# Kernel tuning notes

Hardware: AMD Instinct MI355X
Metric: run time of the kernel (lower is better)

Reference implementation:

```python
import jax, jax.numpy as jnp
import numpy as np

N_NODES = 100000
N_EDGES = 1250000
D_IN = 64
D_H = 64
D_OUT = 32


def setup_inputs() -> dict:
    key = jax.random.key(0)
    ks = jax.random.split(key, 8)
    x = jax.random.normal(ks[0], (N_NODES, D_IN), dtype=jnp.float32)
    edge_index = jax.random.randint(ks[1], (2, N_EDGES), 0, N_NODES, dtype=jnp.int64)
    s = 0.1
    W1_l = jax.random.normal(ks[2], (D_H, D_IN), dtype=jnp.float32) * s
    W1_r = jax.random.normal(ks[3], (D_H, D_IN), dtype=jnp.float32) * s
    b1 = jnp.zeros((D_H,), dtype=jnp.float32)
    W2_l = jax.random.normal(ks[4], (D_OUT, D_H), dtype=jnp.float32) * s
    W2_r = jax.random.normal(ks[5], (D_OUT, D_H), dtype=jnp.float32) * s
    b2 = jnp.zeros((D_OUT,), dtype=jnp.float32)
    return {"x": x, "edge_index": edge_index, "W1_l": W1_l, "W1_r": W1_r,
            "b1": b1, "W2_l": W2_l, "W2_r": W2_r, "b2": b2}


def _sage_conv(x, src, dst, W_l, W_r, b):
    # PyG SAGEConv (aggr='mean', root_weight=True):
    #   out = lin_l(mean_{j in N(i)} x_j) + lin_r(x_i)
    n = x.shape[0]
    msg = x[src]                                            # [E, d] gather
    ssum = jax.ops.segment_sum(msg, dst, num_segments=n)    # [N, d]
    deg = jax.ops.segment_sum(jnp.ones((src.shape[0], 1), x.dtype), dst,
                              num_segments=n)               # [N, 1]
    mean = ssum / jnp.maximum(deg, 1.0)
    return mean @ W_l.T + b + x @ W_r.T


def reference(x, edge_index, W1_l, W1_r, b1, W2_l, W2_r, b2):
    src = edge_index[0]
    dst = edge_index[1]
    h = jax.nn.relu(_sage_conv(x, src, dst, W1_l, W1_r, b1))
    out = _sage_conv(h, src, dst, W2_l, W2_r, b2)
    return out
```

## Files before the change

kernel.cpp:

```cpp
#include <hip/hip_runtime.h>

#define N_NODES 100000
#define N_EDGES 1250000
#define D_IN 64
#define D_H 64
#define D_OUT 32

#define BUCKETS 196
#define GRP 512
#define PREP_NB 512
#define PREP_CH 2442
#define SCAP 48
#define BSTRIDE (PREP_NB*SCAP)
#define CSRCAP 8192

#define XS 6.0f
#define HS 5.0f

typedef __attribute__((ext_vector_type(8))) short bf16x8;
typedef __attribute__((ext_vector_type(4))) float f32x4;

__device__ __forceinline__ unsigned short f2bf(float f) {
    unsigned u = __float_as_uint(f);
    u = (u + 0x7fffu + ((u >> 16) & 1u)) >> 16;
    return (unsigned short)u;
}
__device__ __forceinline__ float bfhi(unsigned v) { return __uint_as_float(v & 0xffff0000u); }
__device__ __forceinline__ float bflo(unsigned v) { return __uint_as_float(v << 16); }


__global__ __launch_bounds__(256) void k_prep(const float* __restrict__ x,
                                              unsigned* __restrict__ xq,
                                              const int* __restrict__ src,
                                              const int* __restrict__ dst,
                                              int* __restrict__ ebuf,
                                              int* __restrict__ pcnt) {
    __shared__ int ofs[BUCKETS];
    int t = threadIdx.x, b = blockIdx.x;
    for (int i = t; i < BUCKETS; i += 256) ofs[i] = 0;
    __syncthreads();

    const float QS = 127.0f / XS;
    const int TOT = N_NODES * 64 / 4;
    for (int i = b * 256 + t; i < TOT; i += PREP_NB * 256) {
        float4 v = *(const float4*)(x + (size_t)i * 4);
        float c0 = fminf(fmaxf(v.x, -XS), XS);
        float c1 = fminf(fmaxf(v.y, -XS), XS);
        float c2 = fminf(fmaxf(v.z, -XS), XS);
        float c3 = fminf(fmaxf(v.w, -XS), XS);
        unsigned q0 = (unsigned)((int)rintf(c0 * QS) + 128);
        unsigned q1 = (unsigned)((int)rintf(c1 * QS) + 128);
        unsigned q2 = (unsigned)((int)rintf(c2 * QS) + 128);
        unsigned q3 = (unsigned)((int)rintf(c3 * QS) + 128);
        xq[i] = q0 | (q1 << 8) | (q2 << 16) | (q3 << 24);
    }

    int e0 = b * PREP_CH;
    int e1 = e0 + PREP_CH; if (e1 > N_EDGES) e1 = N_EDGES;
    for (int e = e0 + t; e < e1; e += 256) {
        int s = src[e], d = dst[e];
        if ((unsigned)d >= N_NODES) continue;
        int sv = ((unsigned)s < N_NODES) ? s : 0;
        int bk = d >> 9;
        int r = atomicAdd(&ofs[bk], 1);
        if (r < SCAP) ebuf[bk * BSTRIDE + b * SCAP + r] = ((d & 511) << 17) | sv;
    }
    __syncthreads();
    for (int i = t; i < BUCKETS; i += 256) {
        int v = ofs[i]; if (v > SCAP) v = SCAP;
        pcnt[i * PREP_NB + b] = v;
    }
}

__global__ __launch_bounds__(512) void k_phb(const int* __restrict__ ebuf,
                                             const int* __restrict__ pcnt,
                                             int2* __restrict__ rd,
                                             int* __restrict__ csr_src) {
    __shared__ int sedge[CSRCAP];
    __shared__ int cnt[GRP];
    __shared__ int wsum[8];
    int b = blockIdx.x, t = threadIdx.x;
    int lane = t & 63, w = t >> 6;

    cnt[t] = 0;
    int c = pcnt[b * PREP_NB + t];

    int run = c;
    #pragma unroll
    for (int off = 1; off < 64; off <<= 1) {
        int u = __shfl_up(run, off, 64);
        if (lane >= off) run += u;
    }
    if (lane == 63) wsum[w] = run;
    __syncthreads();
    int wbase = 0, tot = 0;
    #pragma unroll
    for (int i = 0; i < 8; ++i) { int v = wsum[i]; tot += v; if (i < w) wbase += v; }
    int base = wbase + run - c;
    int n = tot; if (n > CSRCAP) n = CSRCAP;

    {
        const int4* sp4 = (const int4*)(ebuf + (size_t)b * BSTRIDE + (size_t)t * SCAP);
        for (int j = 0; j < c; j += 4) {
            int4 v = sp4[j >> 2];
            int p = base + j;
            if (p + 0 < CSRCAP)              sedge[p + 0] = v.x;
            if (j + 1 < c && p + 1 < CSRCAP) sedge[p + 1] = v.y;
            if (j + 2 < c && p + 2 < CSRCAP) sedge[p + 2] = v.z;
            if (j + 3 < c && p + 3 < CSRCAP) sedge[p + 3] = v.w;
        }
    }
    __syncthreads();
    for (int i = t; i < n; i += 512) atomicAdd(&cnt[sedge[i] >> 17], 1);
    __syncthreads();

    int d = cnt[t];
    int rund = d;
    #pragma unroll
    for (int off = 1; off < 64; off <<= 1) {
        int u = __shfl_up(rund, off, 64);
        if (lane >= off) rund += u;
    }
    if (lane == 63) wsum[w] = rund;
    __syncthreads();
    int wb2 = 0;
    #pragma unroll
    for (int i = 0; i < 8; ++i) { if (i < w) wb2 += wsum[i]; }
    int gabs = b * CSRCAP + wb2 + rund - d;
    int node = b * GRP + t;
    if (node < N_NODES) rd[node] = make_int2(gabs, d);
    cnt[t] = gabs;
    __syncthreads();
    for (int i = t; i < n; i += 512) {
        int v = sedge[i];
        int pos = atomicAdd(&cnt[v >> 17], 1);
        csr_src[pos] = v & 0x1FFFF;
    }
}

__global__ __launch_bounds__(256) void k_gather1(
    const unsigned* __restrict__ xq,
    const int2* __restrict__ rd, const int* __restrict__ csr_src,
    uint4* __restrict__ meanh)
{
    int lane = threadIdx.x & 63;
    int wv = threadIdx.x >> 6;
    int c = lane & 7;
    int gb = lane & 56;
    const uint2* xp = (const uint2*)xq;

    int node0 = blockIdx.x * 32 + wv * 8 + (gb >> 3);
    for (int row = node0; row < N_NODES; row += gridDim.x * 32) {
        int2 rdv = rd[row];
        int start = rdv.x, dg = rdv.y;
        int end = start + dg;
        unsigned aL0=0, aH0=0, aL1=0, aH1=0;
        unsigned bL0=0, bH0=0, bL1=0, bH1=0;
        unsigned cL0=0, cH0=0, cL1=0, cH1=0;
        unsigned dL0=0, dH0=0, dL1=0, dH1=0;
        for (int eb = start; eb < end; eb += 8) {
            int nv = end - eb; if (nv > 8) nv = 8;
            int sid = (c < nv) ? csr_src[eb + c] : 0;
            int j = 0;
            for (; j + 4 <= nv; j += 4) {
                int s0 = __shfl(sid, gb + j + 0, 64);
                int s1 = __shfl(sid, gb + j + 1, 64);
                int s2 = __shfl(sid, gb + j + 2, 64);
                int s3 = __shfl(sid, gb + j + 3, 64);
                uint2 v0 = xp[(size_t)s0 * 8 + c];
                uint2 v1 = xp[(size_t)s1 * 8 + c];
                uint2 v2 = xp[(size_t)s2 * 8 + c];
                uint2 v3 = xp[(size_t)s3 * 8 + c];
                aL0 += v0.x & 0x00FF00FFu; aH0 += (v0.x >> 8) & 0x00FF00FFu;
                aL1 += v0.y & 0x00FF00FFu; aH1 += (v0.y >> 8) & 0x00FF00FFu;
                bL0 += v1.x & 0x00FF00FFu; bH0 += (v1.x >> 8) & 0x00FF00FFu;
                bL1 += v1.y & 0x00FF00FFu; bH1 += (v1.y >> 8) & 0x00FF00FFu;
                cL0 += v2.x & 0x00FF00FFu; cH0 += (v2.x >> 8) & 0x00FF00FFu;
                cL1 += v2.y & 0x00FF00FFu; cH1 += (v2.y >> 8) & 0x00FF00FFu;
                dL0 += v3.x & 0x00FF00FFu; dH0 += (v3.x >> 8) & 0x00FF00FFu;
                dL1 += v3.y & 0x00FF00FFu; dH1 += (v3.y >> 8) & 0x00FF00FFu;
            }
            for (; j < nv; ++j) {
                int s0 = __shfl(sid, gb + j, 64);
                uint2 v0 = xp[(size_t)s0 * 8 + c];
                aL0 += v0.x & 0x00FF00FFu; aH0 += (v0.x >> 8) & 0x00FF00FFu;
                aL1 += v0.y & 0x00FF00FFu; aH1 += (v0.y >> 8) & 0x00FF00FFu;
            }
        }
        unsigned L0 = (aL0 + bL0) + (cL0 + dL0);
        unsigned H0 = (aH0 + bH0) + (cH0 + dH0);
        unsigned L1 = (aL1 + bL1) + (cL1 + dL1);
        unsigned H1 = (aH1 + bH1) + (cH1 + dH1);
        float fd = (float)dg;
        float rdeg = 1.0f / fmaxf(fd, 1.0f);
        const float SC = XS / 127.0f;
        float base = -128.0f * fd;
        float m0 = ((float)(L0 & 0xFFFFu) + base) * SC * rdeg;
        float m1 = ((float)(H0 & 0xFFFFu) + base) * SC * rdeg;
        float m2 = ((float)(L0 >> 16)    + base) * SC * rdeg;
        float m3 = ((float)(H0 >> 16)    + base) * SC * rdeg;
        float m4 = ((float)(L1 & 0xFFFFu) + base) * SC * rdeg;
        float m5 = ((float)(H1 & 0xFFFFu) + base) * SC * rdeg;
        float m6 = ((float)(L1 >> 16)    + base) * SC * rdeg;
        float m7 = ((float)(H1 >> 16)    + base) * SC * rdeg;
        uint4 o;
        o.x = (unsigned)f2bf(m0) | ((unsigned)f2bf(m1) << 16);
        o.y = (unsigned)f2bf(m2) | ((unsigned)f2bf(m3) << 16);
        o.z = (unsigned)f2bf(m4) | ((unsigned)f2bf(m5) << 16);
        o.w = (unsigned)f2bf(m6) | ((unsigned)f2bf(m7) << 16);
        meanh[(size_t)row * 8 + c] = o;
    }
}

__global__ __launch_bounds__(256) void k_gemm1(
    const float* __restrict__ x, const unsigned short* __restrict__ meanh,
    const float* __restrict__ W1l, const float* __restrict__ W1r,
    const float* __restrict__ b1,
    const float* __restrict__ W2l, const float* __restrict__ W2r,
    unsigned char* __restrict__ hq, unsigned short* __restrict__ hrh)
{
    __shared__ short sWB1[4 * 4 * 64 * 8];
    __shared__ short sWB2[2 * 4 * 64 * 8];
    __shared__ short htile[4][16 * 72];

    int tid = threadIdx.x;
    for (int e = tid; e < 1024; e += 256) {
        int kc = e >> 8, nt = (e >> 6) & 3, ln = e & 63;
        int cc = ln & 15, qd = ln >> 4;
        int n = nt * 16 + cc, k0 = kc * 32 + qd * 8;
        const float* sp = (k0 < 64) ? (W1l + n * 64 + k0) : (W1r + n * 64 + (k0 - 64));
        short* dp = sWB1 + e * 8;
        #pragma unroll
        for (int j = 0; j < 8; ++j) dp[j] = (short)f2bf(sp[j]);
    }
    for (int e = tid; e < 512; e += 256) {
        int kc = e >> 8, nt = (e >> 6) & 3, ln = e & 63;
        int cc = ln & 15, qd = ln >> 4;
        int n = nt * 16 + cc, k0 = kc * 32 + qd * 8;
        const float* sp = (n < 32) ? (W2l + n * 64 + k0) : (W2r + (n - 32) * 64 + k0);
        short* dp = sWB2 + e * 8;
        #pragma unroll
        for (int j = 0; j < 8; ++j) dp[j] = (short)f2bf(sp[j]);
    }
    __syncthreads();

    int lane = tid & 63, w = tid >> 6;
    int c = lane & 15, quad = lane >> 4;
    float bias[4];
    #pragma unroll
    for (int nt = 0; nt < 4; ++nt) bias[nt] = b1[nt * 16 + c];

    const bf16x8* B1 = (const bf16x8*)sWB1;
    const bf16x8* B2 = (const bf16x8*)sWB2;
    short* ht = htile[w];
    const float HQS = 127.0f / HS;

    for (int r0 = blockIdx.x * 64 + w * 16; r0 < N_NODES; r0 += gridDim.x * 64) {
        int ra = r0 + c; if (ra > N_NODES - 1) ra = N_NODES - 1;
        const bf16x8* mrow = (const bf16x8*)(meanh + (size_t)ra * 64);
        const float4* xr = (const float4*)(x + (size_t)ra * 64);
        bf16x8 a0 = mrow[quad];
        bf16x8 a1 = mrow[4 + quad];
        float4 f0 = xr[quad * 2 + 0];
        float4 f1 = xr[quad * 2 + 1];
        float4 f2 = xr[8 + quad * 2 + 0];
        float4 f3 = xr[8 + quad * 2 + 1];
        bf16x8 a2, a3;
        a2[0] = (short)f2bf(f0.x); a2[1] = (short)f2bf(f0.y);
        a2[2] = (short)f2bf(f0.z); a2[3] = (short)f2bf(f0.w);
        a2[4] = (short)f2bf(f1.x); a2[5] = (short)f2bf(f1.y);
        a2[6] = (short)f2bf(f1.z); a2[7] = (short)f2bf(f1.w);
        a3[0] = (short)f2bf(f2.x); a3[1] = (short)f2bf(f2.y);
        a3[2] = (short)f2bf(f2.z); a3[3] = (short)f2bf(f2.w);
        a3[4] = (short)f2bf(f3.x); a3[5] = (short)f2bf(f3.y);
        a3[6] = (short)f2bf(f3.z); a3[7] = (short)f2bf(f3.w);

        f32x4 acc[4];
        #pragma unroll
        for (int nt = 0; nt < 4; ++nt) acc[nt] = (f32x4){0.f, 0.f, 0.f, 0.f};
        #pragma unroll
        for (int nt = 0; nt < 4; ++nt)
            acc[nt] = __builtin_amdgcn_mfma_f32_16x16x32_bf16(a0, B1[(0 * 4 + nt) * 64 + lane], acc[nt], 0, 0, 0);
        #pragma unroll
        for (int nt = 0; nt < 4; ++nt)
            acc[nt] = __builtin_amdgcn_mfma_f32_16x16x32_bf16(a1, B1[(1 * 4 + nt) * 64 + lane], acc[nt], 0, 0, 0);
        #pragma unroll
        for (int nt = 0; nt < 4; ++nt)
            acc[nt] = __builtin_amdgcn_mfma_f32_16x16x32_bf16(a2, B1[(2 * 4 + nt) * 64 + lane], acc[nt], 0, 0, 0);
        #pragma unroll
        for (int nt = 0; nt < 4; ++nt)
            acc[nt] = __builtin_amdgcn_mfma_f32_16x16x32_bf16(a3, B1[(3 * 4 + nt) * 64 + lane], acc[nt], 0, 0, 0);

        #pragma unroll
        for (int nt = 0; nt < 4; ++nt) {
            #pragma unroll
            for (int reg = 0; reg < 4; ++reg) {
                float hv = fmaxf(acc[nt][reg] + bias[nt], 0.0f);
                ht[(quad * 4 + reg) * 72 + nt * 16 + c] = (short)f2bf(hv);
            }
        }
        bf16x8 h0 = *(const bf16x8*)(ht + c * 72 + 0  + quad * 8);
        bf16x8 h1 = *(const bf16x8*)(ht + c * 72 + 32 + quad * 8);

        f32x4 acc2[4];
        #pragma unroll
        for (int nt = 0; nt < 4; ++nt) acc2[nt] = (f32x4){0.f, 0.f, 0.f, 0.f};
        #pragma unroll
        for (int nt = 0; nt < 4; ++nt)
            acc2[nt] = __builtin_amdgcn_mfma_f32_16x16x32_bf16(h0, B2[(0 * 4 + nt) * 64 + lane], acc2[nt], 0, 0, 0);
        #pragma unroll
        for (int nt = 0; nt < 4; ++nt)
            acc2[nt] = __builtin_amdgcn_mfma_f32_16x16x32_bf16(h1, B2[(1 * 4 + nt) * 64 + lane], acc2[nt], 0, 0, 0);

        #pragma unroll
        for (int reg = 0; reg < 4; ++reg) {
            int row = r0 + quad * 4 + reg;
            if (row < N_NODES) {
                float c0v = fminf(fmaxf(acc2[0][reg], -HS), HS);
                float c1v = fminf(fmaxf(acc2[1][reg], -HS), HS);
                unsigned q0 = (unsigned)((int)rintf(c0v * HQS) + 128);
                unsigned q1 = (unsigned)((int)rintf(c1v * HQS) + 128);
                hq[(size_t)row * 32 + c]      = (unsigned char)q0;
                hq[(size_t)row * 32 + 16 + c] = (unsigned char)q1;
                hrh[(size_t)row * 32 + c]      = f2bf(acc2[2][reg]);
                hrh[(size_t)row * 32 + 16 + c] = f2bf(acc2[3][reg]);
            }
        }
    }
}

__global__ __launch_bounds__(256) void k_l2(
    const unsigned char* __restrict__ hq,
    const unsigned short* __restrict__ hrh,
    const int2* __restrict__ rd, const int* __restrict__ csr_src,
    const float* __restrict__ b2, float* __restrict__ out)
{
    int lane = threadIdx.x & 63;
    int wv = threadIdx.x >> 6;
    int cc = lane & 3;
    int gb = lane & 60;
    const uint2* hp = (const uint2*)hq;
    const uint4* hrp = (const uint4*)hrh;
    float4 b2v0 = ((const float4*)b2)[cc * 2 + 0];
    float4 b2v1 = ((const float4*)b2)[cc * 2 + 1];

    int node0 = blockIdx.x * 64 + wv * 16 + (gb >> 2);
    for (int row = node0; row < N_NODES; row += gridDim.x * 64) {
        int2 rdv = rd[row];
        int start = rdv.x, dg = rdv.y;
        int end = start + dg;
        unsigned aL0=0, aH0=0, aL1=0, aH1=0;
        unsigned bL0=0, bH0=0, bL1=0, bH1=0;
        unsigned cL0=0, cH0=0, cL1=0, cH1=0;
        unsigned dL0=0, dH0=0, dL1=0, dH1=0;
        for (int eb = start; eb < end; eb += 4) {
            int nv = end - eb; if (nv > 4) nv = 4;
            int sid = (cc < nv) ? csr_src[eb + cc] : 0;
            if (nv == 4) {
                int s0 = __shfl(sid, gb + 0, 64);
                int s1 = __shfl(sid, gb + 1, 64);
                int s2 = __shfl(sid, gb + 2, 64);
                int s3 = __shfl(sid, gb + 3, 64);
                uint2 v0 = hp[(size_t)s0 * 4 + cc];
                uint2 v1 = hp[(size_t)s1 * 4 + cc];
                uint2 v2 = hp[(size_t)s2 * 4 + cc];
                uint2 v3 = hp[(size_t)s3 * 4 + cc];
                aL0 += v0.x & 0x00FF00FFu; aH0 += (v0.x >> 8) & 0x00FF00FFu;
                aL1 += v0.y & 0x00FF00FFu; aH1 += (v0.y >> 8) & 0x00FF00FFu;
                bL0 += v1.x & 0x00FF00FFu; bH0 += (v1.x >> 8) & 0x00FF00FFu;
                bL1 += v1.y & 0x00FF00FFu; bH1 += (v1.y >> 8) & 0x00FF00FFu;
                cL0 += v2.x & 0x00FF00FFu; cH0 += (v2.x >> 8) & 0x00FF00FFu;
                cL1 += v2.y & 0x00FF00FFu; cH1 += (v2.y >> 8) & 0x00FF00FFu;
                dL0 += v3.x & 0x00FF00FFu; dH0 += (v3.x >> 8) & 0x00FF00FFu;
                dL1 += v3.y & 0x00FF00FFu; dH1 += (v3.y >> 8) & 0x00FF00FFu;
            } else {
                for (int j = 0; j < nv; ++j) {
                    int s0 = __shfl(sid, gb + j, 64);
                    uint2 v0 = hp[(size_t)s0 * 4 + cc];
                    aL0 += v0.x & 0x00FF00FFu; aH0 += (v0.x >> 8) & 0x00FF00FFu;
                    aL1 += v0.y & 0x00FF00FFu; aH1 += (v0.y >> 8) & 0x00FF00FFu;
                }
            }
        }
        unsigned L0 = (aL0 + bL0) + (cL0 + dL0);
        unsigned H0 = (aH0 + bH0) + (cH0 + dH0);
        unsigned L1 = (aL1 + bL1) + (cL1 + dL1);
        unsigned H1 = (aH1 + bH1) + (cH1 + dH1);
        float fd = (float)dg;
        float rdeg = 1.0f / fmaxf(fd, 1.0f);
        const float SC = HS / 127.0f;
        float base = -128.0f * fd;
        uint4 hru = hrp[(size_t)row * 4 + cc];
        float4 o0, o1;
        o0.x = ((float)(L0 & 0xFFFFu) + base) * SC * rdeg + (bflo(hru.x) + b2v0.x);
        o0.y = ((float)(H0 & 0xFFFFu) + base) * SC * rdeg + (bfhi(hru.x) + b2v0.y);
        o0.z = ((float)(L0 >> 16)     + base) * SC * rdeg + (bflo(hru.y) + b2v0.z);
        o0.w = ((float)(H0 >> 16)     + base) * SC * rdeg + (bfhi(hru.y) + b2v0.w);
        o1.x = ((float)(L1 & 0xFFFFu) + base) * SC * rdeg + (bflo(hru.z) + b2v1.x);
        o1.y = ((float)(H1 & 0xFFFFu) + base) * SC * rdeg + (bfhi(hru.z) + b2v1.y);
        o1.z = ((float)(L1 >> 16)     + base) * SC * rdeg + (bflo(hru.w) + b2v1.z);
        o1.w = ((float)(H1 >> 16)     + base) * SC * rdeg + (bfhi(hru.w) + b2v1.w);
        ((float4*)out)[(size_t)row * 8 + cc * 2 + 0] = o0;
        ((float4*)out)[(size_t)row * 8 + cc * 2 + 1] = o1;
    }
}

extern "C" void kernel_launch(void* const* d_in, const int* in_sizes, int n_in,
                              void* d_out, int out_size, void* d_ws, size_t ws_size,
                              hipStream_t stream) {
    const float* x   = (const float*)d_in[0];
    const int*   ei  = (const int*)d_in[1];
    const float* W1l = (const float*)d_in[2];
    const float* W1r = (const float*)d_in[3];
    const float* b1  = (const float*)d_in[4];
    const float* W2l = (const float*)d_in[5];
    const float* W2r = (const float*)d_in[6];
    const float* b2  = (const float*)d_in[7];
    float* out = (float*)d_out;

    const int* src = ei;
    const int* dst = ei + N_EDGES;

    char* w = (char*)d_ws;
    int2* rd     = (int2*)w;  w += sizeof(int2) * (N_NODES + 4);
    int* pcnt    = (int*)w;   w += sizeof(int) * (PREP_NB * BUCKETS);
    int* csr_src = (int*)w;   w += sizeof(int) * (BUCKETS * CSRCAP);
    int* ebuf    = (int*)w;   w += sizeof(int) * ((size_t)BUCKETS * BSTRIDE);
    unsigned*       xq   = (unsigned*)w;       w += sizeof(int)   * (size_t)N_NODES * 16;
    unsigned*       meanh  = (unsigned*)w;     w += sizeof(int)   * (size_t)N_NODES * 32;
    unsigned char*  hq   = (unsigned char*)w;  w += (size_t)N_NODES * 32;
    unsigned short* hrh  = (unsigned short*)w;

    k_prep<<<PREP_NB, 256, 0, stream>>>(x, xq, src, dst, ebuf, pcnt);
    k_phb<<<BUCKETS, 512, 0, stream>>>(ebuf, pcnt, rd, csr_src);
    k_gather1<<<3125, 256, 0, stream>>>(xq, rd, csr_src, (uint4*)meanh);
    k_gemm1<<<1024, 256, 0, stream>>>(
        x, (const unsigned short*)meanh, W1l, W1r, b1, W2l, W2r, hq, hrh);
    k_l2<<<1563, 256, 0, stream>>>(hq, hrh, rd, csr_src, b2, out);
}
```

Before: 173.2 us.

## Fuse layer-1 neighbor gather into the layer-1 GEMM kernel via LDS tile

Merges the separate gather kernel into the GEMM kernel. Each wave now gathers the int8 neighbor features for its 16 rows, 4 lanes per row with 16-byte loads, and writes the bf16 mean into its LDS tile, where the MFMA A operands are read. This drops the global round trip for the mean buffer and one kernel launch. In exchange, gather parallelism falls from 3125 blocks to 1024 persistent blocks with fewer loads in flight per row, so latency hiding for the irregular gather may suffer.

```diff
diff --git a/kernel.cpp b/kernel.cpp
--- a/kernel.cpp
+++ b/kernel.cpp
@@ -138,82 +138,9 @@
     }
 }
 
-__global__ __launch_bounds__(256) void k_gather1(
-    const unsigned* __restrict__ xq,
+__global__ __launch_bounds__(256) void k_gg(
+    const float* __restrict__ x, const unsigned* __restrict__ xq,
     const int2* __restrict__ rd, const int* __restrict__ csr_src,
-    uint4* __restrict__ meanh)
-{
-    int lane = threadIdx.x & 63;
-    int wv = threadIdx.x >> 6;
-    int c = lane & 7;
-    int gb = lane & 56;
-    const uint2* xp = (const uint2*)xq;
-
-    int node0 = blockIdx.x * 32 + wv * 8 + (gb >> 3);
-    for (int row = node0; row < N_NODES; row += gridDim.x * 32) {
-        int2 rdv = rd[row];
-        int start = rdv.x, dg = rdv.y;
-        int end = start + dg;
-        unsigned aL0=0, aH0=0, aL1=0, aH1=0;
-        unsigned bL0=0, bH0=0, bL1=0, bH1=0;
-        unsigned cL0=0, cH0=0, cL1=0, cH1=0;
-        unsigned dL0=0, dH0=0, dL1=0, dH1=0;
-        for (int eb = start; eb < end; eb += 8) {
-            int nv = end - eb; if (nv > 8) nv = 8;
-            int sid = (c < nv) ? csr_src[eb + c] : 0;
-            int j = 0;
-            for (; j + 4 <= nv; j += 4) {
-                int s0 = __shfl(sid, gb + j + 0, 64);
-                int s1 = __shfl(sid, gb + j + 1, 64);
-                int s2 = __shfl(sid, gb + j + 2, 64);
-                int s3 = __shfl(sid, gb + j + 3, 64);
-                uint2 v0 = xp[(size_t)s0 * 8 + c];
-                uint2 v1 = xp[(size_t)s1 * 8 + c];
-                uint2 v2 = xp[(size_t)s2 * 8 + c];
-                uint2 v3 = xp[(size_t)s3 * 8 + c];
-                aL0 += v0.x & 0x00FF00FFu; aH0 += (v0.x >> 8) & 0x00FF00FFu;
-                aL1 += v0.y & 0x00FF00FFu; aH1 += (v0.y >> 8) & 0x00FF00FFu;
-                bL0 += v1.x & 0x00FF00FFu; bH0 += (v1.x >> 8) & 0x00FF00FFu;
-                bL1 += v1.y & 0x00FF00FFu; bH1 += (v1.y >> 8) & 0x00FF00FFu;
-                cL0 += v2.x & 0x00FF00FFu; cH0 += (v2.x >> 8) & 0x00FF00FFu;
-                cL1 += v2.y & 0x00FF00FFu; cH1 += (v2.y >> 8) & 0x00FF00FFu;
-                dL0 += v3.x & 0x00FF00FFu; dH0 += (v3.x >> 8) & 0x00FF00FFu;
-                dL1 += v3.y & 0x00FF00FFu; dH1 += (v3.y >> 8) & 0x00FF00FFu;
-            }
-            for (; j < nv; ++j) {
-                int s0 = __shfl(sid, gb + j, 64);
-                uint2 v0 = xp[(size_t)s0 * 8 + c];
-                aL0 += v0.x & 0x00FF00FFu; aH0 += (v0.x >> 8) & 0x00FF00FFu;
-                aL1 += v0.y & 0x00FF00FFu; aH1 += (v0.y >> 8) & 0x00FF00FFu;
-            }
-        }
-        unsigned L0 = (aL0 + bL0) + (cL0 + dL0);
-        unsigned H0 = (aH0 + bH0) + (cH0 + dH0);
-        unsigned L1 = (aL1 + bL1) + (cL1 + dL1);
-        unsigned H1 = (aH1 + bH1) + (cH1 + dH1);
-        float fd = (float)dg;
-        float rdeg = 1.0f / fmaxf(fd, 1.0f);
-        const float SC = XS / 127.0f;
-        float base = -128.0f * fd;
-        float m0 = ((float)(L0 & 0xFFFFu) + base) * SC * rdeg;
-        float m1 = ((float)(H0 & 0xFFFFu) + base) * SC * rdeg;
-        float m2 = ((float)(L0 >> 16)    + base) * SC * rdeg;
-        float m3 = ((float)(H0 >> 16)    + base) * SC * rdeg;
-        float m4 = ((float)(L1 & 0xFFFFu) + base) * SC * rdeg;
-        float m5 = ((float)(H1 & 0xFFFFu) + base) * SC * rdeg;
-        float m6 = ((float)(L1 >> 16)    + base) * SC * rdeg;
-        float m7 = ((float)(H1 >> 16)    + base) * SC * rdeg;
-        uint4 o;
-        o.x = (unsigned)f2bf(m0) | ((unsigned)f2bf(m1) << 16);
-        o.y = (unsigned)f2bf(m2) | ((unsigned)f2bf(m3) << 16);
-        o.z = (unsigned)f2bf(m4) | ((unsigned)f2bf(m5) << 16);
-        o.w = (unsigned)f2bf(m6) | ((unsigned)f2bf(m7) << 16);
-        meanh[(size_t)row * 8 + c] = o;
-    }
-}
-
-__global__ __launch_bounds__(256) void k_gemm1(
-    const float* __restrict__ x, const unsigned short* __restrict__ meanh,
     const float* __restrict__ W1l, const float* __restrict__ W1r,
     const float* __restrict__ b1,
     const float* __restrict__ W2l, const float* __restrict__ W2r,
@@ -246,21 +173,102 @@
 
     int lane = tid & 63, w = tid >> 6;
     int c = lane & 15, quad = lane >> 4;
+    int gl = lane & 3, gb = lane & 60, gr = lane >> 2;
     float bias[4];
     #pragma unroll
     for (int nt = 0; nt < 4; ++nt) bias[nt] = b1[nt * 16 + c];
 
     const bf16x8* B1 = (const bf16x8*)sWB1;
     const bf16x8* B2 = (const bf16x8*)sWB2;
+    const uint4* xp4 = (const uint4*)xq;
     short* ht = htile[w];
     const float HQS = 127.0f / HS;
+    const float SC = XS / 127.0f;
 
     for (int r0 = blockIdx.x * 64 + w * 16; r0 < N_NODES; r0 += gridDim.x * 64) {
+        {
+            int grow = r0 + gr;
+            int2 rdv = rd[(grow < N_NODES) ? grow : (N_NODES - 1)];
+            int start = rdv.x;
+            int dg = (grow < N_NODES) ? rdv.y : 0;
+            int end = start + dg;
+            unsigned L0=0,H0=0,L1=0,H1=0,L2=0,H2=0,L3=0,H3=0;
+            for (int eb = start; eb < end; eb += 4) {
+                int nv = end - eb; if (nv > 4) nv = 4;
+                int sid = (gl < nv) ? csr_src[eb + gl] : 0;
+                if (nv == 4) {
+                    int s0 = __shfl(sid, gb + 0, 64);
+                    int s1 = __shfl(sid, gb + 1, 64);
+                    int s2 = __shfl(sid, gb + 2, 64);
+                    int s3 = __shfl(sid, gb + 3, 64);
+                    uint4 v0 = xp4[(size_t)s0 * 4 + gl];
+                    uint4 v1 = xp4[(size_t)s1 * 4 + gl];
+                    uint4 v2 = xp4[(size_t)s2 * 4 + gl];
+                    uint4 v3 = xp4[(size_t)s3 * 4 + gl];
+                    L0 += v0.x & 0x00FF00FFu; H0 += (v0.x >> 8) & 0x00FF00FFu;
+                    L1 += v0.y & 0x00FF00FFu; H1 += (v0.y >> 8) & 0x00FF00FFu;
+                    L2 += v0.z & 0x00FF00FFu; H2 += (v0.z >> 8) & 0x00FF00FFu;
+                    L3 += v0.w & 0x00FF00FFu; H3 += (v0.w >> 8) & 0x00FF00FFu;
+                    L0 += v1.x & 0x00FF00FFu; H0 += (v1.x >> 8) & 0x00FF00FFu;
+                    L1 += v1.y & 0x00FF00FFu; H1 += (v1.y >> 8) & 0x00FF00FFu;
+                    L2 += v1.z & 0x00FF00FFu; H2 += (v1.z >> 8) & 0x00FF00FFu;
+                    L3 += v1.w & 0x00FF00FFu; H3 += (v1.w >> 8) & 0x00FF00FFu;
+                    L0 += v2.x & 0x00FF00FFu; H0 += (v2.x >> 8) & 0x00FF00FFu;
+                    L1 += v2.y & 0x00FF00FFu; H1 += (v2.y >> 8) & 0x00FF00FFu;
+                    L2 += v2.z & 0x00FF00FFu; H2 += (v2.z >> 8) & 0x00FF00FFu;
+                    L3 += v2.w & 0x00FF00FFu; H3 += (v2.w >> 8) & 0x00FF00FFu;
+                    L0 += v3.x & 0x00FF00FFu; H0 += (v3.x >> 8) & 0x00FF00FFu;
+                    L1 += v3.y & 0x00FF00FFu; H1 += (v3.y >> 8) & 0x00FF00FFu;
+                    L2 += v3.z & 0x00FF00FFu; H2 += (v3.z >> 8) & 0x00FF00FFu;
+                    L3 += v3.w & 0x00FF00FFu; H3 += (v3.w >> 8) & 0x00FF00FFu;
+                } else {
+                    for (int j = 0; j < nv; ++j) {
+                        int s0 = __shfl(sid, gb + j, 64);
+                        uint4 v0 = xp4[(size_t)s0 * 4 + gl];
+                        L0 += v0.x & 0x00FF00FFu; H0 += (v0.x >> 8) & 0x00FF00FFu;
+                        L1 += v0.y & 0x00FF00FFu; H1 += (v0.y >> 8) & 0x00FF00FFu;
+                        L2 += v0.z & 0x00FF00FFu; H2 += (v0.z >> 8) & 0x00FF00FFu;
+                        L3 += v0.w & 0x00FF00FFu; H3 += (v0.w >> 8) & 0x00FF00FFu;
+                    }
+                }
+            }
+            float fd = (float)dg;
+            float rdeg = 1.0f / fmaxf(fd, 1.0f);
+            float base = -128.0f * fd;
+            float m0  = ((float)(L0 & 0xFFFFu) + base) * SC * rdeg;
+            float m1  = ((float)(H0 & 0xFFFFu) + base) * SC * rdeg;
+            float m2  = ((float)(L0 >> 16)     + base) * SC * rdeg;
+            float m3  = ((float)(H0 >> 16)     + base) * SC * rdeg;
+            float m4  = ((float)(L1 & 0xFFFFu) + base) * SC * rdeg;
+            float m5  = ((float)(H1 & 0xFFFFu) + base) * SC * rdeg;
+            float m6  = ((float)(L1 >> 16)     + base) * SC * rdeg;
+            float m7  = ((float)(H1 >> 16)     + base) * SC * rdeg;
+            float m8  = ((float)(L2 & 0xFFFFu) + base) * SC * rdeg;
+            float m9  = ((float)(H2 & 0xFFFFu) + base) * SC * rdeg;
+            float m10 = ((float)(L2 >> 16)     + base) * SC * rdeg;
+            float m11 = ((float)(H2 >> 16)     + base) * SC * rdeg;
+            float m12 = ((float)(L3 & 0xFFFFu) + base) * SC * rdeg;
+            float m13 = ((float)(H3 & 0xFFFFu) + base) * SC * rdeg;
+            float m14 = ((float)(L3 >> 16)     + base) * SC * rdeg;
+            float m15 = ((float)(H3 >> 16)     + base) * SC * rdeg;
+            uint4 o0, o1;
+            o0.x = (unsigned)f2bf(m0)  | ((unsigned)f2bf(m1)  << 16);
+            o0.y = (unsigned)f2bf(m2)  | ((unsigned)f2bf(m3)  << 16);
+            o0.z = (unsigned)f2bf(m4)  | ((unsigned)f2bf(m5)  << 16);
+            o0.w = (unsigned)f2bf(m6)  | ((unsigned)f2bf(m7)  << 16);
+            o1.x = (unsigned)f2bf(m8)  | ((unsigned)f2bf(m9)  << 16);
+            o1.y = (unsigned)f2bf(m10) | ((unsigned)f2bf(m11) << 16);
+            o1.z = (unsigned)f2bf(m12) | ((unsigned)f2bf(m13) << 16);
+            o1.w = (unsigned)f2bf(m14) | ((unsigned)f2bf(m15) << 16);
+            uint4* hw = (uint4*)(ht + gr * 72 + gl * 16);
+            hw[0] = o0;
+            hw[1] = o1;
+        }
+
         int ra = r0 + c; if (ra > N_NODES - 1) ra = N_NODES - 1;
-        const bf16x8* mrow = (const bf16x8*)(meanh + (size_t)ra * 64);
+        bf16x8 a0 = *(const bf16x8*)(ht + c * 72 + 0  + quad * 8);
+        bf16x8 a1 = *(const bf16x8*)(ht + c * 72 + 32 + quad * 8);
         const float4* xr = (const float4*)(x + (size_t)ra * 64);
-        bf16x8 a0 = mrow[quad];
-        bf16x8 a1 = mrow[4 + quad];
         float4 f0 = xr[quad * 2 + 0];
         float4 f1 = xr[quad * 2 + 1];
         float4 f2 = xr[8 + quad * 2 + 0];
@@ -427,14 +435,12 @@
     int* csr_src = (int*)w;   w += sizeof(int) * (BUCKETS * CSRCAP);
     int* ebuf    = (int*)w;   w += sizeof(int) * ((size_t)BUCKETS * BSTRIDE);
     unsigned*       xq   = (unsigned*)w;       w += sizeof(int)   * (size_t)N_NODES * 16;
-    unsigned*       meanh  = (unsigned*)w;     w += sizeof(int)   * (size_t)N_NODES * 32;
     unsigned char*  hq   = (unsigned char*)w;  w += (size_t)N_NODES * 32;
     unsigned short* hrh  = (unsigned short*)w;
 
     k_prep<<<PREP_NB, 256, 0, stream>>>(x, xq, src, dst, ebuf, pcnt);
     k_phb<<<BUCKETS, 512, 0, stream>>>(ebuf, pcnt, rd, csr_src);
-    k_gather1<<<3125, 256, 0, stream>>>(xq, rd, csr_src, (uint4*)meanh);
-    k_gemm1<<<1024, 256, 0, stream>>>(
-        x, (const unsigned short*)meanh, W1l, W1r, b1, W2l, W2r, hq, hrh);
+    k_gg<<<1024, 256, 0, stream>>>(
+        x, xq, rd, csr_src, W1l, W1r, b1, W2l, W2r, hq, hrh);
     k_l2<<<1563, 256, 0, stream>>>(hq, hrh, rd, csr_src, b2, out);
 }
```

Result: slower. 182.4 us (+5.3%).
